# Kernel tuning notes

Measured on AMD Instinct MI355X. Metric: run time of the kernel, lower is better.

## Reference

```python
import jax, jax.numpy as jnp
import numpy as np

N, E = 50000, 800000
D_IN, D_H, D_OUT, N_LAYERS = 3, 64, 128, 3


def setup_inputs() -> dict:
    key = jax.random.key(0)
    ks = jax.random.split(key, 16)
    s = lambda k, shape, fan: jax.random.normal(k, shape, jnp.float32) * (1.0 / np.sqrt(fan))
    return {
        "x": jax.random.normal(ks[0], (N, D_IN), jnp.float32),
        "edge_index": jax.random.randint(ks[1], (2, E), 0, N, jnp.int32),
        "in_w": s(ks[2], (D_IN, D_H), D_IN),
        "in_b": jnp.zeros((D_H,), jnp.float32),
        "msg_w1": s(ks[3], (N_LAYERS, 2 * D_H, D_H), 2 * D_H),
        "msg_b1": jnp.zeros((N_LAYERS, D_H), jnp.float32),
        "msg_w2": s(ks[4], (N_LAYERS, D_H, D_H), D_H),
        "msg_b2": jnp.zeros((N_LAYERS, D_H), jnp.float32),
        "upd_w1": s(ks[5], (N_LAYERS, 2 * D_H, D_H), 2 * D_H),
        "upd_b1": jnp.zeros((N_LAYERS, D_H), jnp.float32),
        "upd_w2": s(ks[6], (N_LAYERS, D_H, D_H), D_H),
        "upd_b2": jnp.zeros((N_LAYERS, D_H), jnp.float32),
        "out_w": s(ks[7], (D_H, D_OUT), D_H),
        "out_b": jnp.zeros((D_OUT,), jnp.float32),
    }


def reference(x, edge_index, in_w, in_b, msg_w1, msg_b1, msg_w2, msg_b2,
              upd_w1, upd_b1, upd_w2, upd_b2, out_w, out_b):
    row, col = edge_index[0], edge_index[1]
    h = x @ in_w + in_b  # [N, D_H]
    for l in range(N_LAYERS):
        # gather-concat-MLP message: [E, 2*D_H] -> [E, D_H]
        msg_in = jnp.concatenate([h[row], h[col]], axis=-1)
        m = jax.nn.relu(msg_in @ msg_w1[l] + msg_b1[l]) @ msg_w2[l] + msg_b2[l]
        # scatter-add aggregation into destination nodes
        agg = jax.ops.segment_sum(m, col, num_segments=N)  # [N, D_H]
        # update MLP on concat(node, aggregated)
        upd_in = jnp.concatenate([h, agg], axis=-1)
        u = jax.nn.relu(upd_in @ upd_w1[l] + upd_b1[l]) @ upd_w2[l] + upd_b2[l]
        h = jax.nn.relu(u)
    return h @ out_w + out_b  # [N, D_OUT]
```

## Files before the change

### kernel.cpp

```cpp
#include <hip/hip_runtime.h>
#include <hip/hip_bf16.h>

#define NN 50000
#define NE 800000

typedef __bf16 bf16_t;
typedef unsigned short u16;
typedef bf16_t bf16x4 __attribute__((ext_vector_type(4)));
typedef bf16_t bf16x8 __attribute__((ext_vector_type(8)));
typedef float f32x4 __attribute__((ext_vector_type(4)));

__device__ __forceinline__ bf16x8 load_frag(const bf16_t* p) {
    bf16x4 lo = *(const bf16x4*)p;
    bf16x4 hi = *(const bf16x4*)(p + 16);
    bf16x8 f;
    f[0] = lo[0]; f[1] = lo[1]; f[2] = lo[2]; f[3] = lo[3];
    f[4] = hi[0]; f[5] = hi[1]; f[6] = hi[2]; f[7] = hi[3];
    return f;
}

__device__ __forceinline__ bf16x8 load_frag2(const bf16_t* p, const bf16_t* q) {
    bf16x8 a = load_frag(p);
    bf16x8 b = load_frag(q);
    bf16x8 f;
    #pragma unroll
    for (int j = 0; j < 8; ++j) f[j] = (bf16_t)((float)a[j] + (float)b[j]);
    return f;
}

__global__ void k_prepall(const float* __restrict__ mw1, const float* __restrict__ uw1,
                          const float* __restrict__ uw2,
                          const float* __restrict__ mw2, const float* __restrict__ mb2,
                          const float* __restrict__ ow,
                          bf16_t* __restrict__ w1t, bf16_t* __restrict__ u1t,
                          bf16_t* __restrict__ u2t,
                          bf16_t* __restrict__ w2u, float* __restrict__ cvec,
                          bf16_t* __restrict__ whi, bf16_t* __restrict__ wlo,
                          int* __restrict__ deg) {
    int gid = blockIdx.x * blockDim.x + threadIdx.x;
    int nthr = gridDim.x * blockDim.x;
    for (int i = gid; i < NN; i += nthr) deg[i] = 0;
    if (gid < 3 * 64 * 128) {
        int l = gid / 8192, r = gid % 8192, hid = r >> 7, k = r & 127;
        w1t[gid] = (bf16_t)mw1[l * 8192 + k * 64 + hid];
    }
    if (gid < 3 * 64 * 64) {
        int l = gid / 4096, r = gid % 4096, hid = r >> 6, k = r & 63;
        u1t[gid] = (bf16_t)uw1[l * 8192 + k * 64 + hid];
        u2t[gid] = (bf16_t)uw2[l * 4096 + k * 64 + hid];
        float s = 0.f;
        for (int j = 0; j < 64; ++j)
            s += mw2[l * 4096 + k * 64 + j] * uw1[l * 8192 + (64 + j) * 64 + hid];
        w2u[l * 4096 + hid * 64 + k] = (bf16_t)s;
    }
    if (gid < 3 * 64) {
        int l = gid / 64, hid = gid % 64;
        float s = 0.f;
        for (int j = 0; j < 64; ++j)
            s += mb2[l * 64 + j] * uw1[l * 8192 + (64 + j) * 64 + hid];
        cvec[gid] = s;
    }
    if (gid < 128 * 64) {
        int j = gid >> 6, k = gid & 63;
        float w = ow[k * 128 + j];
        bf16_t hi = (bf16_t)w;
        whi[gid] = hi;
        wlo[gid] = (bf16_t)(w - (float)hi);
    }
}

__global__ void k_hist(const int* __restrict__ ei, int* __restrict__ deg) {
    int gid = blockIdx.x * blockDim.x + threadIdx.x;
    if (gid < NE) atomicAdd(&deg[ei[NE + gid]], 1);
}

#define SCAN_BLKS 196
__global__ void k_scan1(const int* __restrict__ deg, int* __restrict__ tscan,
                        int* __restrict__ part) {
    __shared__ int lds[256];
    int tid = threadIdx.x;
    int gid = blockIdx.x * 256 + tid;
    int v = (gid < NN) ? deg[gid] : 0;
    lds[tid] = v;
    __syncthreads();
    for (int off = 1; off < 256; off <<= 1) {
        int t = (tid >= off) ? lds[tid - off] : 0;
        __syncthreads();
        lds[tid] += t;
        __syncthreads();
    }
    if (gid < NN) tscan[gid] = lds[tid] - v;
    if (tid == 255) part[blockIdx.x] = lds[255];
}

__global__ void k_scan23(const int* __restrict__ tscan, const int* __restrict__ part,
                         int* __restrict__ offs, int* __restrict__ cursor) {
    __shared__ int lds[256];
    int tid = threadIdx.x;
    int v = (tid < SCAN_BLKS) ? part[tid] : 0;
    lds[tid] = v;
    __syncthreads();
    for (int off = 1; off < 256; off <<= 1) {
        int t = (tid >= off) ? lds[tid - off] : 0;
        __syncthreads();
        lds[tid] += t;
        __syncthreads();
    }
    __shared__ int base;
    if (tid == 0) base = (blockIdx.x > 0) ? lds[blockIdx.x - 1] : 0;
    __syncthreads();
    int gid = blockIdx.x * 256 + tid;
    if (gid < NN) {
        int o = tscan[gid] + base;
        offs[gid] = o;
        cursor[gid] = o;
    }
    if (gid == 0) offs[NN] = NE;
}

__global__ void k_scatter(const int* __restrict__ ei, int* __restrict__ cursor,
                          u16* __restrict__ ssrc) {
    int gid = blockIdx.x * blockDim.x + threadIdx.x;
    if (gid < NE) {
        int c = ei[NE + gid];
        int pos = atomicAdd(&cursor[c], 1);
        ssrc[pos] = (u16)ei[gid];
    }
}

__global__ __launch_bounds__(256)
void k_inputpq(const float* __restrict__ x, const float* __restrict__ iw,
               const float* __restrict__ ib,
               const bf16_t* __restrict__ w1t, const float* __restrict__ b1,
               bf16_t* __restrict__ h, bf16_t* __restrict__ P, bf16_t* __restrict__ Q) {
    const int lane = threadIdx.x & 63;
    const int g = lane >> 4;
    const int m16 = lane & 15;
    const int wid = (blockIdx.x * blockDim.x + threadIdx.x) >> 6;
    const int nw = (gridDim.x * blockDim.x) >> 6;

    bf16x8 wtop[2][4], wbot[2][4];
    #pragma unroll
    for (int s = 0; s < 2; ++s)
        #pragma unroll
        for (int nt = 0; nt < 4; ++nt) {
            wtop[s][nt] = load_frag(w1t + (16 * nt + m16) * 128 + 32 * s + 4 * g);
            wbot[s][nt] = load_frag(w1t + (16 * nt + m16) * 128 + 64 + 32 * s + 4 * g);
        }
    float b1f[4][4];
    #pragma unroll
    for (int nt = 0; nt < 4; ++nt)
        #pragma unroll
        for (int r = 0; r < 4; ++r) b1f[nt][r] = b1[16 * nt + 4 * g + r];

    float wcol[3][2][8], bcol[2][8];
    #pragma unroll
    for (int s = 0; s < 2; ++s)
        #pragma unroll
        for (int j = 0; j < 8; ++j) {
            int f = 32 * s + 4 * g + (j < 4 ? j : 16 + j - 4);
            bcol[s][j] = ib[f];
            #pragma unroll
            for (int i = 0; i < 3; ++i) wcol[i][s][j] = iw[i * 64 + f];
        }

    const int ntiles = NN / 16;
    for (int t = wid; t < ntiles; t += nw) {
        const int node = t * 16 + m16;
        float x0 = x[node * 3 + 0], x1 = x[node * 3 + 1], x2 = x[node * 3 + 2];
        bf16x8 hb[2];
        #pragma unroll
        for (int s = 0; s < 2; ++s)
            #pragma unroll
            for (int j = 0; j < 8; ++j) {
                float hf = bcol[s][j] + x0 * wcol[0][s][j] + x1 * wcol[1][s][j]
                         + x2 * wcol[2][s][j];
                hb[s][j] = (bf16_t)hf;
            }
        #pragma unroll
        for (int s = 0; s < 2; ++s) {
            bf16x4 lo, hi;
            #pragma unroll
            for (int j = 0; j < 4; ++j) { lo[j] = hb[s][j]; hi[j] = hb[s][4 + j]; }
            *(bf16x4*)(h + node * 64 + 32 * s + 4 * g) = lo;
            *(bf16x4*)(h + node * 64 + 32 * s + 16 + 4 * g) = hi;
        }

        f32x4 accP[4], accQ[4];
        #pragma unroll
        for (int nt = 0; nt < 4; ++nt) {
            accP[nt] = (f32x4){0.f, 0.f, 0.f, 0.f};
            accQ[nt] = (f32x4){0.f, 0.f, 0.f, 0.f};
        }
        #pragma unroll
        for (int s = 0; s < 2; ++s)
            #pragma unroll
            for (int nt = 0; nt < 4; ++nt) {
                accP[nt] = __builtin_amdgcn_mfma_f32_16x16x32_bf16(wtop[s][nt], hb[s], accP[nt], 0, 0, 0);
                accQ[nt] = __builtin_amdgcn_mfma_f32_16x16x32_bf16(wbot[s][nt], hb[s], accQ[nt], 0, 0, 0);
            }
        #pragma unroll
        for (int nt = 0; nt < 4; ++nt) {
            bf16x4 vp, vq;
            #pragma unroll
            for (int r = 0; r < 4; ++r) {
                vp[r] = (bf16_t)accP[nt][r];
                vq[r] = (bf16_t)(accQ[nt][r] + b1f[nt][r]);
            }
            *(bf16x4*)(P + node * 64 + 16 * nt + 4 * g) = vp;
            *(bf16x4*)(Q + node * 64 + 16 * nt + 4 * g) = vq;
        }
    }
}

__global__ void k_edge(const bf16_t* __restrict__ P, const bf16_t* __restrict__ Q,
                       const u16* __restrict__ ssrc, const int* __restrict__ offs,
                       bf16_t* __restrict__ S, bf16_t* __restrict__ S2) {
    int gid = blockIdx.x * blockDim.x + threadIdx.x;
    int oct = gid >> 3, f8 = gid & 7;
    int node = oct >> 1, half = oct & 1;
    if (node >= NN) return;
    bf16x8 qv = *(const bf16x8*)(Q + node * 64 + f8 * 8);
    float qf[8], a[8];
    #pragma unroll
    for (int r = 0; r < 8; ++r) { qf[r] = (float)qv[r]; a[r] = 0.f; }
    const int b0 = offs[node], e0 = offs[node + 1];
    const int mid = b0 + ((e0 - b0 + 1) >> 1);
    const int beg = half ? mid : b0;
    const int end = half ? e0 : mid;
    int p = beg;
    const int n4 = beg + ((end - beg) & ~3);
    for (; p < n4; p += 4) {
        int s0 = ssrc[p], s1 = ssrc[p + 1], s2 = ssrc[p + 2], s3 = ssrc[p + 3];
        bf16x8 v0 = *(const bf16x8*)(P + s0 * 64 + f8 * 8);
        bf16x8 v1 = *(const bf16x8*)(P + s1 * 64 + f8 * 8);
        bf16x8 v2 = *(const bf16x8*)(P + s2 * 64 + f8 * 8);
        bf16x8 v3 = *(const bf16x8*)(P + s3 * 64 + f8 * 8);
        #pragma unroll
        for (int r = 0; r < 8; ++r) {
            float x0 = (float)v0[r] + qf[r];
            float x1 = (float)v1[r] + qf[r];
            float x2 = (float)v2[r] + qf[r];
            float x3 = (float)v3[r] + qf[r];
            a[r] += (x0 > 0.f ? x0 : 0.f) + (x1 > 0.f ? x1 : 0.f)
                  + (x2 > 0.f ? x2 : 0.f) + (x3 > 0.f ? x3 : 0.f);
        }
    }
    for (; p < end; ++p) {
        int s = ssrc[p];
        bf16x8 v = *(const bf16x8*)(P + s * 64 + f8 * 8);
        #pragma unroll
        for (int r = 0; r < 8; ++r) {
            float x = (float)v[r] + qf[r];
            a[r] += x > 0.f ? x : 0.f;
        }
    }
    bf16x8 sv;
    #pragma unroll
    for (int r = 0; r < 8; ++r) sv[r] = (bf16_t)a[r];
    bf16_t* dst = half ? S2 : S;
    *(bf16x8*)(dst + node * 64 + f8 * 8) = sv;
}

__global__ __launch_bounds__(256)
void k_updpq(const bf16_t* __restrict__ h, const bf16_t* __restrict__ S,
             const bf16_t* __restrict__ S2, const int* __restrict__ deg,
             const bf16_t* __restrict__ u1t, const bf16_t* __restrict__ w2u,
             const bf16_t* __restrict__ u2t,
             const float* __restrict__ ub1, const float* __restrict__ cvec,
             const float* __restrict__ ub2,
             const bf16_t* __restrict__ w1tn, const float* __restrict__ b1n,
             bf16_t* __restrict__ hn, bf16_t* __restrict__ P, bf16_t* __restrict__ Q) {
    const int lane = threadIdx.x & 63;
    const int g = lane >> 4;
    const int m16 = lane & 15;
    const int wid = (blockIdx.x * blockDim.x + threadIdx.x) >> 6;
    const int nw = (gridDim.x * blockDim.x) >> 6;

    bf16x8 u1f[2][4], w2f[2][4], u2f[2][4], wtop[2][4], wbot[2][4];
    #pragma unroll
    for (int s = 0; s < 2; ++s)
        #pragma unroll
        for (int nt = 0; nt < 4; ++nt) {
            u1f[s][nt] = load_frag(u1t + (16 * nt + m16) * 64 + 32 * s + 4 * g);
            w2f[s][nt] = load_frag(w2u + (16 * nt + m16) * 64 + 32 * s + 4 * g);
            u2f[s][nt] = load_frag(u2t + (16 * nt + m16) * 64 + 32 * s + 4 * g);
            wtop[s][nt] = load_frag(w1tn + (16 * nt + m16) * 128 + 32 * s + 4 * g);
            wbot[s][nt] = load_frag(w1tn + (16 * nt + m16) * 128 + 64 + 32 * s + 4 * g);
        }
    float b1f[4][4], cf[4][4], b2f[4][4], b1nf[4][4];
    #pragma unroll
    for (int nt = 0; nt < 4; ++nt)
        #pragma unroll
        for (int r = 0; r < 4; ++r) {
            b1f[nt][r] = ub1[16 * nt + 4 * g + r];
            cf[nt][r] = cvec[16 * nt + 4 * g + r];
            b2f[nt][r] = ub2[16 * nt + 4 * g + r];
            b1nf[nt][r] = b1n[16 * nt + 4 * g + r];
        }

    const int ntiles = NN / 16;
    for (int t = wid; t < ntiles; t += nw) {
        const int node = t * 16 + m16;
        bf16x8 hfr[2], sfr[2];
        hfr[0] = load_frag(h + node * 64 + 4 * g);
        hfr[1] = load_frag(h + node * 64 + 4 * g + 32);
        sfr[0] = load_frag2(S + node * 64 + 4 * g, S2 + node * 64 + 4 * g);
        sfr[1] = load_frag2(S + node * 64 + 4 * g + 32, S2 + node * 64 + 4 * g + 32);
        float dv = (float)deg[node];

        f32x4 acc1[4];
        #pragma unroll
        for (int nt = 0; nt < 4; ++nt) acc1[nt] = (f32x4){0.f, 0.f, 0.f, 0.f};
        #pragma unroll
        for (int s = 0; s < 2; ++s)
            #pragma unroll
            for (int nt = 0; nt < 4; ++nt) {
                acc1[nt] = __builtin_amdgcn_mfma_f32_16x16x32_bf16(u1f[s][nt], hfr[s], acc1[nt], 0, 0, 0);
                acc1[nt] = __builtin_amdgcn_mfma_f32_16x16x32_bf16(w2f[s][nt], sfr[s], acc1[nt], 0, 0, 0);
            }

        bf16x8 hb[2];
        #pragma unroll
        for (int s = 0; s < 2; ++s) {
            bf16x8 f;
            #pragma unroll
            for (int half = 0; half < 2; ++half) {
                const int nt = 2 * s + half;
                #pragma unroll
                for (int r = 0; r < 4; ++r) {
                    float v = acc1[nt][r] + b1f[nt][r] + dv * cf[nt][r];
                    v = v > 0.f ? v : 0.f;
                    f[4 * half + r] = (bf16_t)v;
                }
            }
            hb[s] = f;
        }

        f32x4 acc2[4];
        #pragma unroll
        for (int nt = 0; nt < 4; ++nt) acc2[nt] = (f32x4){0.f, 0.f, 0.f, 0.f};
        #pragma unroll
        for (int s = 0; s < 2; ++s)
            #pragma unroll
            for (int nt = 0; nt < 4; ++nt)
                acc2[nt] = __builtin_amdgcn_mfma_f32_16x16x32_bf16(u2f[s][nt], hb[s], acc2[nt], 0, 0, 0);

        bf16x8 hb2[2];
        #pragma unroll
        for (int s = 0; s < 2; ++s) {
            bf16x8 f;
            #pragma unroll
            for (int half = 0; half < 2; ++half) {
                const int nt = 2 * s + half;
                #pragma unroll
                for (int r = 0; r < 4; ++r) {
                    float v = acc2[nt][r] + b2f[nt][r];
                    f[4 * half + r] = (bf16_t)(v > 0.f ? v : 0.f);
                }
            }
            hb2[s] = f;
        }
        #pragma unroll
        for (int s = 0; s < 2; ++s) {
            bf16x4 lo, hi;
            #pragma unroll
            for (int j = 0; j < 4; ++j) { lo[j] = hb2[s][j]; hi[j] = hb2[s][4 + j]; }
            *(bf16x4*)(hn + node * 64 + 32 * s + 4 * g) = lo;
            *(bf16x4*)(hn + node * 64 + 32 * s + 16 + 4 * g) = hi;
        }

        f32x4 accP[4], accQ[4];
        #pragma unroll
        for (int nt = 0; nt < 4; ++nt) {
            accP[nt] = (f32x4){0.f, 0.f, 0.f, 0.f};
            accQ[nt] = (f32x4){0.f, 0.f, 0.f, 0.f};
        }
        #pragma unroll
        for (int s = 0; s < 2; ++s)
            #pragma unroll
            for (int nt = 0; nt < 4; ++nt) {
                accP[nt] = __builtin_amdgcn_mfma_f32_16x16x32_bf16(wtop[s][nt], hb2[s], accP[nt], 0, 0, 0);
                accQ[nt] = __builtin_amdgcn_mfma_f32_16x16x32_bf16(wbot[s][nt], hb2[s], accQ[nt], 0, 0, 0);
            }
        #pragma unroll
        for (int nt = 0; nt < 4; ++nt) {
            bf16x4 vp, vq;
            #pragma unroll
            for (int r = 0; r < 4; ++r) {
                vp[r] = (bf16_t)accP[nt][r];
                vq[r] = (bf16_t)(accQ[nt][r] + b1nf[nt][r]);
            }
            *(bf16x4*)(P + node * 64 + 16 * nt + 4 * g) = vp;
            *(bf16x4*)(Q + node * 64 + 16 * nt + 4 * g) = vq;
        }
    }
}

__global__ void k_upd(const bf16_t* __restrict__ h, const bf16_t* __restrict__ S,
                      const bf16_t* __restrict__ S2, const int* __restrict__ deg,
                      const bf16_t* __restrict__ u1t, const bf16_t* __restrict__ w2u,
                      const bf16_t* __restrict__ u2t,
                      const float* __restrict__ ub1, const float* __restrict__ cvec,
                      const float* __restrict__ ub2, bf16_t* __restrict__ hn) {
    const int lane = threadIdx.x & 63;
    const int g = lane >> 4;
    const int m16 = lane & 15;
    const int wid = (blockIdx.x * blockDim.x + threadIdx.x) >> 6;
    const int nw = (gridDim.x * blockDim.x) >> 6;

    bf16x8 u1f[2][4], w2f[2][4], u2f[2][4];
    #pragma unroll
    for (int s = 0; s < 2; ++s)
        #pragma unroll
        for (int nt = 0; nt < 4; ++nt) {
            u1f[s][nt] = load_frag(u1t + (16 * nt + m16) * 64 + 32 * s + 4 * g);
            w2f[s][nt] = load_frag(w2u + (16 * nt + m16) * 64 + 32 * s + 4 * g);
            u2f[s][nt] = load_frag(u2t + (16 * nt + m16) * 64 + 32 * s + 4 * g);
        }
    float b1f[4][4], cf[4][4], b2f[4][4];
    #pragma unroll
    for (int nt = 0; nt < 4; ++nt)
        #pragma unroll
        for (int r = 0; r < 4; ++r) {
            b1f[nt][r] = ub1[16 * nt + 4 * g + r];
            cf[nt][r] = cvec[16 * nt + 4 * g + r];
            b2f[nt][r] = ub2[16 * nt + 4 * g + r];
        }

    const int ntiles = NN / 16;
    for (int t = wid; t < ntiles; t += nw) {
        const int node = t * 16 + m16;
        bf16x8 hfr[2], sfr[2];
        hfr[0] = load_frag(h + node * 64 + 4 * g);
        hfr[1] = load_frag(h + node * 64 + 4 * g + 32);
        sfr[0] = load_frag2(S + node * 64 + 4 * g, S2 + node * 64 + 4 * g);
        sfr[1] = load_frag2(S + node * 64 + 4 * g + 32, S2 + node * 64 + 4 * g + 32);
        float dv = (float)deg[node];

        f32x4 acc1[4];
        #pragma unroll
        for (int nt = 0; nt < 4; ++nt) acc1[nt] = (f32x4){0.f, 0.f, 0.f, 0.f};
        #pragma unroll
        for (int s = 0; s < 2; ++s)
            #pragma unroll
            for (int nt = 0; nt < 4; ++nt) {
                acc1[nt] = __builtin_amdgcn_mfma_f32_16x16x32_bf16(u1f[s][nt], hfr[s], acc1[nt], 0, 0, 0);
                acc1[nt] = __builtin_amdgcn_mfma_f32_16x16x32_bf16(w2f[s][nt], sfr[s], acc1[nt], 0, 0, 0);
            }

        bf16x8 hb[2];
        #pragma unroll
        for (int s = 0; s < 2; ++s) {
            bf16x8 f;
            #pragma unroll
            for (int half = 0; half < 2; ++half) {
                const int nt = 2 * s + half;
                #pragma unroll
                for (int r = 0; r < 4; ++r) {
                    float v = acc1[nt][r] + b1f[nt][r] + dv * cf[nt][r];
                    v = v > 0.f ? v : 0.f;
                    f[4 * half + r] = (bf16_t)v;
                }
            }
            hb[s] = f;
        }

        f32x4 acc2[4];
        #pragma unroll
        for (int nt = 0; nt < 4; ++nt) acc2[nt] = (f32x4){0.f, 0.f, 0.f, 0.f};
        #pragma unroll
        for (int s = 0; s < 2; ++s)
            #pragma unroll
            for (int nt = 0; nt < 4; ++nt)
                acc2[nt] = __builtin_amdgcn_mfma_f32_16x16x32_bf16(u2f[s][nt], hb[s], acc2[nt], 0, 0, 0);

        #pragma unroll
        for (int nt = 0; nt < 4; ++nt) {
            bf16x4 v4;
            #pragma unroll
            for (int r = 0; r < 4; ++r) {
                float v = acc2[nt][r] + b2f[nt][r];
                v4[r] = (bf16_t)(v > 0.f ? v : 0.f);
            }
            *(bf16x4*)(hn + node * 64 + 16 * nt + 4 * g) = v4;
        }
    }
}

__global__ __launch_bounds__(256)
void k_outm(const bf16_t* __restrict__ whi_t, const bf16_t* __restrict__ wlo_t,
            const bf16_t* __restrict__ h, const float* __restrict__ b,
            float* __restrict__ out) {
    const int lane = threadIdx.x & 63;
    const int g = lane >> 4;
    const int m16 = lane & 15;
    const int wid = (blockIdx.x * blockDim.x + threadIdx.x) >> 6;
    const int nw = (gridDim.x * blockDim.x) >> 6;

    bf16x8 whi[2][8], wlo[2][8];
    #pragma unroll
    for (int s = 0; s < 2; ++s)
        #pragma unroll
        for (int nt = 0; nt < 8; ++nt) {
            whi[s][nt] = load_frag(whi_t + (16 * nt + m16) * 64 + 32 * s + 4 * g);
            wlo[s][nt] = load_frag(wlo_t + (16 * nt + m16) * 64 + 32 * s + 4 * g);
        }
    f32x4 bfv[8];
    #pragma unroll
    for (int nt = 0; nt < 8; ++nt)
        #pragma unroll
        for (int r = 0; r < 4; ++r) bfv[nt][r] = b[16 * nt + 4 * g + r];

    const int ntiles = NN / 16;
    for (int t = wid; t < ntiles; t += nw) {
        const int node = t * 16 + m16;
        bf16x8 hfr[2];
        hfr[0] = load_frag(h + node * 64 + 4 * g);
        hfr[1] = load_frag(h + node * 64 + 4 * g + 32);

        f32x4 acc[8];
        #pragma unroll
        for (int nt = 0; nt < 8; ++nt) acc[nt] = (f32x4){0.f, 0.f, 0.f, 0.f};
        #pragma unroll
        for (int s = 0; s < 2; ++s)
            #pragma unroll
            for (int nt = 0; nt < 8; ++nt) {
                acc[nt] = __builtin_amdgcn_mfma_f32_16x16x32_bf16(whi[s][nt], hfr[s], acc[nt], 0, 0, 0);
                acc[nt] = __builtin_amdgcn_mfma_f32_16x16x32_bf16(wlo[s][nt], hfr[s], acc[nt], 0, 0, 0);
            }
        #pragma unroll
        for (int nt = 0; nt < 8; ++nt)
            *(f32x4*)(out + node * 128 + 16 * nt + 4 * g) = acc[nt] + bfv[nt];
    }
}

extern "C" void kernel_launch(void* const* d_in, const int* in_sizes, int n_in,
                              void* d_out, int out_size, void* d_ws, size_t ws_size,
                              hipStream_t stream) {
    const float* x      = (const float*)d_in[0];
    const int*   ei     = (const int*)d_in[1];
    const float* in_w   = (const float*)d_in[2];
    const float* in_b   = (const float*)d_in[3];
    const float* msg_w1 = (const float*)d_in[4];
    const float* msg_b1 = (const float*)d_in[5];
    const float* msg_w2 = (const float*)d_in[6];
    const float* msg_b2 = (const float*)d_in[7];
    const float* upd_w1 = (const float*)d_in[8];
    const float* upd_b1 = (const float*)d_in[9];
    const float* upd_w2 = (const float*)d_in[10];
    const float* upd_b2 = (const float*)d_in[11];
    const float* out_w  = (const float*)d_in[12];
    const float* out_b  = (const float*)d_in[13];
    float* out = (float*)d_out;

    char* ws = (char*)d_ws;
    bf16_t* h_a    = (bf16_t*)(ws);
    bf16_t* h_b    = (bf16_t*)(ws + 6400000);
    bf16_t* P      = (bf16_t*)(ws + 12800000);
    bf16_t* Q      = (bf16_t*)(ws + 19200000);
    bf16_t* S      = (bf16_t*)(ws + 25600000);
    u16*    ssrc   = (u16*)   (ws + 32000000);
    int*    deg    = (int*)   (ws + 35200000);
    int*    offs   = (int*)   (ws + 35400000);
    int*    cursor = (int*)   (ws + 35600128);
    int*    tscan  = (int*)   (ws + 35800192);
    int*    part   = (int*)   (ws + 36000256);
    bf16_t* w1t    = (bf16_t*)(ws + 36002304);
    bf16_t* u1t    = (bf16_t*)(ws + 36051456);
    bf16_t* u2t    = (bf16_t*)(ws + 36076032);
    bf16_t* w2u    = (bf16_t*)(ws + 36100608);
    float*  cvec   = (float*) (ws + 36125184);
    bf16_t* whi    = (bf16_t*)(ws + 36126208);
    bf16_t* wlo    = (bf16_t*)(ws + 36142592);
    bf16_t* S2     = (bf16_t*)(ws + 36160000);

    k_prepall<<<96, 256, 0, stream>>>(msg_w1, upd_w1, upd_w2, msg_w2, msg_b2, out_w,
                                      w1t, u1t, u2t, w2u, cvec, whi, wlo, deg);

    k_hist<<<(NE + 255) / 256, 256, 0, stream>>>(ei, deg);
    k_scan1<<<SCAN_BLKS, 256, 0, stream>>>(deg, tscan, part);
    k_scan23<<<SCAN_BLKS, 256, 0, stream>>>(tscan, part, offs, cursor);
    k_scatter<<<(NE + 255) / 256, 256, 0, stream>>>(ei, cursor, ssrc);

    k_inputpq<<<512, 256, 0, stream>>>(x, in_w, in_b, w1t, msg_b1, h_a, P, Q);

    bf16_t* hc = h_a;
    bf16_t* hn = h_b;
    for (int l = 0; l < 3; ++l) {
        k_edge<<<(NN * 16 + 255) / 256, 256, 0, stream>>>(P, Q, ssrc, offs, S, S2);
        if (l < 2) {
            k_updpq<<<512, 256, 0, stream>>>(hc, S, S2, deg,
                u1t + l * 4096, w2u + l * 4096, u2t + l * 4096,
                upd_b1 + l * 64, cvec + l * 64, upd_b2 + l * 64,
                w1t + (l + 1) * 8192, msg_b1 + (l + 1) * 64,
                hn, P, Q);
        } else {
            k_upd<<<512, 256, 0, stream>>>(hc, S, S2, deg,
                u1t + l * 4096, w2u + l * 4096, u2t + l * 4096,
                upd_b1 + l * 64, cvec + l * 64, upd_b2 + l * 64, hn);
        }
        bf16_t* tmp = hc; hc = hn; hn = tmp;
    }
    k_outm<<<640, 256, 0, stream>>>(whi, wlo, hc, out_b, out);
}
```

Baseline: 375.5 us.

## Fuse edge aggregation into per-block update kernel via shared memory

Merges the per-node edge gather/ReLU/sum kernel with the update MLP kernel. Each 256-thread block aggregates 64 nodes into an LDS tile, then runs the MFMA update and next-layer P/Q projection on that tile. P and Q are double-buffered to avoid read/write hazards. This removes the S/S2 global round trip and one launch per layer. In exchange, each node's edges are handled by 4 threads instead of 16, weight fragments are reloaded per block, and imbalanced degrees can stall the MFMA phase.

```diff
diff --git a/kernel.cpp b/kernel.cpp
--- a/kernel.cpp
+++ b/kernel.cpp
@@ -16,15 +16,6 @@
     bf16x8 f;
     f[0] = lo[0]; f[1] = lo[1]; f[2] = lo[2]; f[3] = lo[3];
     f[4] = hi[0]; f[5] = hi[1]; f[6] = hi[2]; f[7] = hi[3];
-    return f;
-}
-
-__device__ __forceinline__ bf16x8 load_frag2(const bf16_t* p, const bf16_t* q) {
-    bf16x8 a = load_frag(p);
-    bf16x8 b = load_frag(q);
-    bf16x8 f;
-    #pragma unroll
-    for (int j = 0; j < 8; ++j) f[j] = (bf16_t)((float)a[j] + (float)b[j]);
     return f;
 }
 
@@ -213,69 +204,79 @@
     }
 }
 
-__global__ void k_edge(const bf16_t* __restrict__ P, const bf16_t* __restrict__ Q,
-                       const u16* __restrict__ ssrc, const int* __restrict__ offs,
-                       bf16_t* __restrict__ S, bf16_t* __restrict__ S2) {
-    int gid = blockIdx.x * blockDim.x + threadIdx.x;
-    int oct = gid >> 3, f8 = gid & 7;
-    int node = oct >> 1, half = oct & 1;
-    if (node >= NN) return;
-    bf16x8 qv = *(const bf16x8*)(Q + node * 64 + f8 * 8);
-    float qf[8], a[8];
-    #pragma unroll
-    for (int r = 0; r < 8; ++r) { qf[r] = (float)qv[r]; a[r] = 0.f; }
-    const int b0 = offs[node], e0 = offs[node + 1];
-    const int mid = b0 + ((e0 - b0 + 1) >> 1);
-    const int beg = half ? mid : b0;
-    const int end = half ? e0 : mid;
-    int p = beg;
-    const int n4 = beg + ((end - beg) & ~3);
-    for (; p < n4; p += 4) {
-        int s0 = ssrc[p], s1 = ssrc[p + 1], s2 = ssrc[p + 2], s3 = ssrc[p + 3];
-        bf16x8 v0 = *(const bf16x8*)(P + s0 * 64 + f8 * 8);
-        bf16x8 v1 = *(const bf16x8*)(P + s1 * 64 + f8 * 8);
-        bf16x8 v2 = *(const bf16x8*)(P + s2 * 64 + f8 * 8);
-        bf16x8 v3 = *(const bf16x8*)(P + s3 * 64 + f8 * 8);
-        #pragma unroll
-        for (int r = 0; r < 8; ++r) {
-            float x0 = (float)v0[r] + qf[r];
-            float x1 = (float)v1[r] + qf[r];
-            float x2 = (float)v2[r] + qf[r];
-            float x3 = (float)v3[r] + qf[r];
-            a[r] += (x0 > 0.f ? x0 : 0.f) + (x1 > 0.f ? x1 : 0.f)
-                  + (x2 > 0.f ? x2 : 0.f) + (x3 > 0.f ? x3 : 0.f);
-        }
-    }
-    for (; p < end; ++p) {
-        int s = ssrc[p];
-        bf16x8 v = *(const bf16x8*)(P + s * 64 + f8 * 8);
-        #pragma unroll
-        for (int r = 0; r < 8; ++r) {
-            float x = (float)v[r] + qf[r];
-            a[r] += x > 0.f ? x : 0.f;
-        }
-    }
-    bf16x8 sv;
-    #pragma unroll
-    for (int r = 0; r < 8; ++r) sv[r] = (bf16_t)a[r];
-    bf16_t* dst = half ? S2 : S;
-    *(bf16x8*)(dst + node * 64 + f8 * 8) = sv;
-}
-
 __global__ __launch_bounds__(256)
-void k_updpq(const bf16_t* __restrict__ h, const bf16_t* __restrict__ S,
-             const bf16_t* __restrict__ S2, const int* __restrict__ deg,
+void k_layer(const bf16_t* __restrict__ h, const bf16_t* __restrict__ P,
+             const bf16_t* __restrict__ Q,
+             const u16* __restrict__ ssrc, const int* __restrict__ offs,
+             const int* __restrict__ deg,
              const bf16_t* __restrict__ u1t, const bf16_t* __restrict__ w2u,
              const bf16_t* __restrict__ u2t,
              const float* __restrict__ ub1, const float* __restrict__ cvec,
              const float* __restrict__ ub2,
              const bf16_t* __restrict__ w1tn, const float* __restrict__ b1n,
-             bf16_t* __restrict__ hn, bf16_t* __restrict__ P, bf16_t* __restrict__ Q) {
-    const int lane = threadIdx.x & 63;
+             const int do_pq,
+             bf16_t* __restrict__ hn, bf16_t* __restrict__ Pn, bf16_t* __restrict__ Qn) {
+    __shared__ float Sl[64][67];
+    const int tid = threadIdx.x;
+
+    {
+        const int nl = tid >> 2;
+        const int f2 = tid & 3;
+        const int node = blockIdx.x * 64 + nl;
+        float qf[16], a[16];
+        #pragma unroll
+        for (int r = 0; r < 16; ++r) a[r] = 0.f;
+        if (node < NN) {
+            bf16x8 q0 = *(const bf16x8*)(Q + node * 64 + f2 * 16);
+            bf16x8 q1 = *(const bf16x8*)(Q + node * 64 + f2 * 16 + 8);
+            #pragma unroll
+            for (int r = 0; r < 8; ++r) { qf[r] = (float)q0[r]; qf[8 + r] = (float)q1[r]; }
+            const int beg = offs[node], end = offs[node + 1];
+            int p = beg;
+            const int n2 = beg + ((end - beg) & ~1);
+            for (; p < n2; p += 2) {
+                int s0 = ssrc[p], s1 = ssrc[p + 1];
+                const bf16_t* p0 = P + s0 * 64 + f2 * 16;
+                const bf16_t* p1 = P + s1 * 64 + f2 * 16;
+                bf16x8 v00 = *(const bf16x8*)p0;
+                bf16x8 v01 = *(const bf16x8*)(p0 + 8);
+                bf16x8 v10 = *(const bf16x8*)p1;
+                bf16x8 v11 = *(const bf16x8*)(p1 + 8);
+                #pragma unroll
+                for (int r = 0; r < 8; ++r) {
+                    float x0 = (float)v00[r] + qf[r];
+                    float x1 = (float)v10[r] + qf[r];
+                    float y0 = (float)v01[r] + qf[8 + r];
+                    float y1 = (float)v11[r] + qf[8 + r];
+                    a[r]     += (x0 > 0.f ? x0 : 0.f) + (x1 > 0.f ? x1 : 0.f);
+                    a[8 + r] += (y0 > 0.f ? y0 : 0.f) + (y1 > 0.f ? y1 : 0.f);
+                }
+            }
+            for (; p < end; ++p) {
+                int s = ssrc[p];
+                const bf16_t* pp = P + s * 64 + f2 * 16;
+                bf16x8 v0 = *(const bf16x8*)pp;
+                bf16x8 v1 = *(const bf16x8*)(pp + 8);
+                #pragma unroll
+                for (int r = 0; r < 8; ++r) {
+                    float x = (float)v0[r] + qf[r];
+                    float y = (float)v1[r] + qf[8 + r];
+                    a[r]     += x > 0.f ? x : 0.f;
+                    a[8 + r] += y > 0.f ? y : 0.f;
+                }
+            }
+        }
+        #pragma unroll
+        for (int r = 0; r < 16; ++r) Sl[nl][f2 * 16 + r] = a[r];
+    }
+    __syncthreads();
+
+    const int lane = tid & 63;
+    const int w = tid >> 6;
     const int g = lane >> 4;
     const int m16 = lane & 15;
-    const int wid = (blockIdx.x * blockDim.x + threadIdx.x) >> 6;
-    const int nw = (gridDim.x * blockDim.x) >> 6;
+    const int nl2 = w * 16 + m16;
+    const int node = blockIdx.x * 64 + nl2;
 
     bf16x8 u1f[2][4], w2f[2][4], u2f[2][4], wtop[2][4], wbot[2][4];
     #pragma unroll
@@ -285,9 +286,16 @@
             u1f[s][nt] = load_frag(u1t + (16 * nt + m16) * 64 + 32 * s + 4 * g);
             w2f[s][nt] = load_frag(w2u + (16 * nt + m16) * 64 + 32 * s + 4 * g);
             u2f[s][nt] = load_frag(u2t + (16 * nt + m16) * 64 + 32 * s + 4 * g);
-            wtop[s][nt] = load_frag(w1tn + (16 * nt + m16) * 128 + 32 * s + 4 * g);
-            wbot[s][nt] = load_frag(w1tn + (16 * nt + m16) * 128 + 64 + 32 * s + 4 * g);
-        }
+        }
+    if (do_pq) {
+        #pragma unroll
+        for (int s = 0; s < 2; ++s)
+            #pragma unroll
+            for (int nt = 0; nt < 4; ++nt) {
+                wtop[s][nt] = load_frag(w1tn + (16 * nt + m16) * 128 + 32 * s + 4 * g);
+                wbot[s][nt] = load_frag(w1tn + (16 * nt + m16) * 128 + 64 + 32 * s + 4 * g);
+            }
+    }
     float b1f[4][4], cf[4][4], b2f[4][4], b1nf[4][4];
     #pragma unroll
     for (int nt = 0; nt < 4; ++nt)
@@ -296,71 +304,77 @@
             b1f[nt][r] = ub1[16 * nt + 4 * g + r];
             cf[nt][r] = cvec[16 * nt + 4 * g + r];
             b2f[nt][r] = ub2[16 * nt + 4 * g + r];
-            b1nf[nt][r] = b1n[16 * nt + 4 * g + r];
-        }
-
-    const int ntiles = NN / 16;
-    for (int t = wid; t < ntiles; t += nw) {
-        const int node = t * 16 + m16;
-        bf16x8 hfr[2], sfr[2];
-        hfr[0] = load_frag(h + node * 64 + 4 * g);
-        hfr[1] = load_frag(h + node * 64 + 4 * g + 32);
-        sfr[0] = load_frag2(S + node * 64 + 4 * g, S2 + node * 64 + 4 * g);
-        sfr[1] = load_frag2(S + node * 64 + 4 * g + 32, S2 + node * 64 + 4 * g + 32);
-        float dv = (float)deg[node];
-
-        f32x4 acc1[4];
-        #pragma unroll
-        for (int nt = 0; nt < 4; ++nt) acc1[nt] = (f32x4){0.f, 0.f, 0.f, 0.f};
-        #pragma unroll
-        for (int s = 0; s < 2; ++s)
-            #pragma unroll
-            for (int nt = 0; nt < 4; ++nt) {
-                acc1[nt] = __builtin_amdgcn_mfma_f32_16x16x32_bf16(u1f[s][nt], hfr[s], acc1[nt], 0, 0, 0);
-                acc1[nt] = __builtin_amdgcn_mfma_f32_16x16x32_bf16(w2f[s][nt], sfr[s], acc1[nt], 0, 0, 0);
-            }
-
-        bf16x8 hb[2];
-        #pragma unroll
-        for (int s = 0; s < 2; ++s) {
-            bf16x8 f;
-            #pragma unroll
-            for (int half = 0; half < 2; ++half) {
-                const int nt = 2 * s + half;
-                #pragma unroll
-                for (int r = 0; r < 4; ++r) {
-                    float v = acc1[nt][r] + b1f[nt][r] + dv * cf[nt][r];
-                    v = v > 0.f ? v : 0.f;
-                    f[4 * half + r] = (bf16_t)v;
-                }
-            }
-            hb[s] = f;
-        }
-
-        f32x4 acc2[4];
-        #pragma unroll
-        for (int nt = 0; nt < 4; ++nt) acc2[nt] = (f32x4){0.f, 0.f, 0.f, 0.f};
-        #pragma unroll
-        for (int s = 0; s < 2; ++s)
-            #pragma unroll
-            for (int nt = 0; nt < 4; ++nt)
-                acc2[nt] = __builtin_amdgcn_mfma_f32_16x16x32_bf16(u2f[s][nt], hb[s], acc2[nt], 0, 0, 0);
-
-        bf16x8 hb2[2];
-        #pragma unroll
-        for (int s = 0; s < 2; ++s) {
-            bf16x8 f;
-            #pragma unroll
-            for (int half = 0; half < 2; ++half) {
-                const int nt = 2 * s + half;
-                #pragma unroll
-                for (int r = 0; r < 4; ++r) {
-                    float v = acc2[nt][r] + b2f[nt][r];
-                    f[4 * half + r] = (bf16_t)(v > 0.f ? v : 0.f);
-                }
-            }
-            hb2[s] = f;
-        }
+            b1nf[nt][r] = do_pq ? b1n[16 * nt + 4 * g + r] : 0.f;
+        }
+
+    bf16x8 hfr[2], sfr[2];
+    hfr[0] = load_frag(h + node * 64 + 4 * g);
+    hfr[1] = load_frag(h + node * 64 + 4 * g + 32);
+    #pragma unroll
+    for (int s = 0; s < 2; ++s) {
+        bf16x8 f;
+        #pragma unroll
+        for (int j = 0; j < 4; ++j) {
+            f[j]     = (bf16_t)Sl[nl2][32 * s + 4 * g + j];
+            f[4 + j] = (bf16_t)Sl[nl2][32 * s + 16 + 4 * g + j];
+        }
+        sfr[s] = f;
+    }
+    float dv = (float)deg[node < NN ? node : 0];
+
+    f32x4 acc1[4];
+    #pragma unroll
+    for (int nt = 0; nt < 4; ++nt) acc1[nt] = (f32x4){0.f, 0.f, 0.f, 0.f};
+    #pragma unroll
+    for (int s = 0; s < 2; ++s)
+        #pragma unroll
+        for (int nt = 0; nt < 4; ++nt) {
+            acc1[nt] = __builtin_amdgcn_mfma_f32_16x16x32_bf16(u1f[s][nt], hfr[s], acc1[nt], 0, 0, 0);
+            acc1[nt] = __builtin_amdgcn_mfma_f32_16x16x32_bf16(w2f[s][nt], sfr[s], acc1[nt], 0, 0, 0);
+        }
+
+    bf16x8 hb[2];
+    #pragma unroll
+    for (int s = 0; s < 2; ++s) {
+        bf16x8 f;
+        #pragma unroll
+        for (int half = 0; half < 2; ++half) {
+            const int nt = 2 * s + half;
+            #pragma unroll
+            for (int r = 0; r < 4; ++r) {
+                float v = acc1[nt][r] + b1f[nt][r] + dv * cf[nt][r];
+                v = v > 0.f ? v : 0.f;
+                f[4 * half + r] = (bf16_t)v;
+            }
+        }
+        hb[s] = f;
+    }
+
+    f32x4 acc2[4];
+    #pragma unroll
+    for (int nt = 0; nt < 4; ++nt) acc2[nt] = (f32x4){0.f, 0.f, 0.f, 0.f};
+    #pragma unroll
+    for (int s = 0; s < 2; ++s)
+        #pragma unroll
+        for (int nt = 0; nt < 4; ++nt)
+            acc2[nt] = __builtin_amdgcn_mfma_f32_16x16x32_bf16(u2f[s][nt], hb[s], acc2[nt], 0, 0, 0);
+
+    bf16x8 hb2[2];
+    #pragma unroll
+    for (int s = 0; s < 2; ++s) {
+        bf16x8 f;
+        #pragma unroll
+        for (int half = 0; half < 2; ++half) {
+            const int nt = 2 * s + half;
+            #pragma unroll
+            for (int r = 0; r < 4; ++r) {
+                float v = acc2[nt][r] + b2f[nt][r];
+                f[4 * half + r] = (bf16_t)(v > 0.f ? v : 0.f);
+            }
+        }
+        hb2[s] = f;
+    }
+    if (node < NN) {
         #pragma unroll
         for (int s = 0; s < 2; ++s) {
             bf16x4 lo, hi;
@@ -369,7 +383,9 @@
             *(bf16x4*)(hn + node * 64 + 32 * s + 4 * g) = lo;
             *(bf16x4*)(hn + node * 64 + 32 * s + 16 + 4 * g) = hi;
         }
-
+    }
+
+    if (do_pq) {
         f32x4 accP[4], accQ[4];
         #pragma unroll
         for (int nt = 0; nt < 4; ++nt) {
@@ -383,107 +399,18 @@
                 accP[nt] = __builtin_amdgcn_mfma_f32_16x16x32_bf16(wtop[s][nt], hb2[s], accP[nt], 0, 0, 0);
                 accQ[nt] = __builtin_amdgcn_mfma_f32_16x16x32_bf16(wbot[s][nt], hb2[s], accQ[nt], 0, 0, 0);
             }
-        #pragma unroll
-        for (int nt = 0; nt < 4; ++nt) {
-            bf16x4 vp, vq;
-            #pragma unroll
-            for (int r = 0; r < 4; ++r) {
-                vp[r] = (bf16_t)accP[nt][r];
-                vq[r] = (bf16_t)(accQ[nt][r] + b1nf[nt][r]);
-            }
-            *(bf16x4*)(P + node * 64 + 16 * nt + 4 * g) = vp;
-            *(bf16x4*)(Q + node * 64 + 16 * nt + 4 * g) = vq;
-        }
-    }
-}
-
-__global__ void k_upd(const bf16_t* __restrict__ h, const bf16_t* __restrict__ S,
-                      const bf16_t* __restrict__ S2, const int* __restrict__ deg,
-                      const bf16_t* __restrict__ u1t, const bf16_t* __restrict__ w2u,
-                      const bf16_t* __restrict__ u2t,
-                      const float* __restrict__ ub1, const float* __restrict__ cvec,
-                      const float* __restrict__ ub2, bf16_t* __restrict__ hn) {
-    const int lane = threadIdx.x & 63;
-    const int g = lane >> 4;
-    const int m16 = lane & 15;
-    const int wid = (blockIdx.x * blockDim.x + threadIdx.x) >> 6;
-    const int nw = (gridDim.x * blockDim.x) >> 6;
-
-    bf16x8 u1f[2][4], w2f[2][4], u2f[2][4];
-    #pragma unroll
-    for (int s = 0; s < 2; ++s)
-        #pragma unroll
-        for (int nt = 0; nt < 4; ++nt) {
-            u1f[s][nt] = load_frag(u1t + (16 * nt + m16) * 64 + 32 * s + 4 * g);
-            w2f[s][nt] = load_frag(w2u + (16 * nt + m16) * 64 + 32 * s + 4 * g);
-            u2f[s][nt] = load_frag(u2t + (16 * nt + m16) * 64 + 32 * s + 4 * g);
-        }
-    float b1f[4][4], cf[4][4], b2f[4][4];
-    #pragma unroll
-    for (int nt = 0; nt < 4; ++nt)
-        #pragma unroll
-        for (int r = 0; r < 4; ++r) {
-            b1f[nt][r] = ub1[16 * nt + 4 * g + r];
-            cf[nt][r] = cvec[16 * nt + 4 * g + r];
-            b2f[nt][r] = ub2[16 * nt + 4 * g + r];
-        }
-
-    const int ntiles = NN / 16;
-    for (int t = wid; t < ntiles; t += nw) {
-        const int node = t * 16 + m16;
-        bf16x8 hfr[2], sfr[2];
-        hfr[0] = load_frag(h + node * 64 + 4 * g);
-        hfr[1] = load_frag(h + node * 64 + 4 * g + 32);
-        sfr[0] = load_frag2(S + node * 64 + 4 * g, S2 + node * 64 + 4 * g);
-        sfr[1] = load_frag2(S + node * 64 + 4 * g + 32, S2 + node * 64 + 4 * g + 32);
-        float dv = (float)deg[node];
-
-        f32x4 acc1[4];
-        #pragma unroll
-        for (int nt = 0; nt < 4; ++nt) acc1[nt] = (f32x4){0.f, 0.f, 0.f, 0.f};
-        #pragma unroll
-        for (int s = 0; s < 2; ++s)
+        if (node < NN) {
             #pragma unroll
             for (int nt = 0; nt < 4; ++nt) {
-                acc1[nt] = __builtin_amdgcn_mfma_f32_16x16x32_bf16(u1f[s][nt], hfr[s], acc1[nt], 0, 0, 0);
-                acc1[nt] = __builtin_amdgcn_mfma_f32_16x16x32_bf16(w2f[s][nt], sfr[s], acc1[nt], 0, 0, 0);
-            }
-
-        bf16x8 hb[2];
-        #pragma unroll
-        for (int s = 0; s < 2; ++s) {
-            bf16x8 f;
-            #pragma unroll
-            for (int half = 0; half < 2; ++half) {
-                const int nt = 2 * s + half;
+                bf16x4 vp, vq;
                 #pragma unroll
                 for (int r = 0; r < 4; ++r) {
-                    float v = acc1[nt][r] + b1f[nt][r] + dv * cf[nt][r];
-                    v = v > 0.f ? v : 0.f;
-                    f[4 * half + r] = (bf16_t)v;
+                    vp[r] = (bf16_t)accP[nt][r];
+                    vq[r] = (bf16_t)(accQ[nt][r] + b1nf[nt][r]);
                 }
-            }
-            hb[s] = f;
-        }
-
-        f32x4 acc2[4];
-        #pragma unroll
-        for (int nt = 0; nt < 4; ++nt) acc2[nt] = (f32x4){0.f, 0.f, 0.f, 0.f};
-        #pragma unroll
-        for (int s = 0; s < 2; ++s)
-            #pragma unroll
-            for (int nt = 0; nt < 4; ++nt)
-                acc2[nt] = __builtin_amdgcn_mfma_f32_16x16x32_bf16(u2f[s][nt], hb[s], acc2[nt], 0, 0, 0);
-
-        #pragma unroll
-        for (int nt = 0; nt < 4; ++nt) {
-            bf16x4 v4;
-            #pragma unroll
-            for (int r = 0; r < 4; ++r) {
-                float v = acc2[nt][r] + b2f[nt][r];
-                v4[r] = (bf16_t)(v > 0.f ? v : 0.f);
-            }
-            *(bf16x4*)(hn + node * 64 + 16 * nt + 4 * g) = v4;
+                *(bf16x4*)(Pn + node * 64 + 16 * nt + 4 * g) = vp;
+                *(bf16x4*)(Qn + node * 64 + 16 * nt + 4 * g) = vq;
+            }
         }
     }
 }
@@ -557,9 +484,9 @@
     char* ws = (char*)d_ws;
     bf16_t* h_a    = (bf16_t*)(ws);
     bf16_t* h_b    = (bf16_t*)(ws + 6400000);
-    bf16_t* P      = (bf16_t*)(ws + 12800000);
-    bf16_t* Q      = (bf16_t*)(ws + 19200000);
-    bf16_t* S      = (bf16_t*)(ws + 25600000);
+    bf16_t* Pa     = (bf16_t*)(ws + 12800000);
+    bf16_t* Qa     = (bf16_t*)(ws + 19200000);
+    bf16_t* Pb     = (bf16_t*)(ws + 25600000);
     u16*    ssrc   = (u16*)   (ws + 32000000);
     int*    deg    = (int*)   (ws + 35200000);
     int*    offs   = (int*)   (ws + 35400000);
@@ -573,7 +500,7 @@
     float*  cvec   = (float*) (ws + 36125184);
     bf16_t* whi    = (bf16_t*)(ws + 36126208);
     bf16_t* wlo    = (bf16_t*)(ws + 36142592);
-    bf16_t* S2     = (bf16_t*)(ws + 36160000);
+    bf16_t* Qb     = (bf16_t*)(ws + 36160000);
 
     k_prepall<<<96, 256, 0, stream>>>(msg_w1, upd_w1, upd_w2, msg_w2, msg_b2, out_w,
                                       w1t, u1t, u2t, w2u, cvec, whi, wlo, deg);
@@ -583,24 +510,24 @@
     k_scan23<<<SCAN_BLKS, 256, 0, stream>>>(tscan, part, offs, cursor);
     k_scatter<<<(NE + 255) / 256, 256, 0, stream>>>(ei, cursor, ssrc);
 
-    k_inputpq<<<512, 256, 0, stream>>>(x, in_w, in_b, w1t, msg_b1, h_a, P, Q);
-
-    bf16_t* hc = h_a;
-    bf16_t* hn = h_b;
+    k_inputpq<<<512, 256, 0, stream>>>(x, in_w, in_b, w1t, msg_b1, h_a, Pa, Qa);
+
+    const int NB = (NN + 63) / 64;
+    bf16_t* hc = h_a; bf16_t* hn = h_b;
+    bf16_t* Pc = Pa;  bf16_t* Qc = Qa;
+    bf16_t* Pn = Pb;  bf16_t* Qn = Qb;
     for (int l = 0; l < 3; ++l) {
-        k_edge<<<(NN * 16 + 255) / 256, 256, 0, stream>>>(P, Q, ssrc, offs, S, S2);
-        if (l < 2) {
-            k_updpq<<<512, 256, 0, stream>>>(hc, S, S2, deg,
-                u1t + l * 4096, w2u + l * 4096, u2t + l * 4096,
-                upd_b1 + l * 64, cvec + l * 64, upd_b2 + l * 64,
-                w1t + (l + 1) * 8192, msg_b1 + (l + 1) * 64,
-                hn, P, Q);
-        } else {
-            k_upd<<<512, 256, 0, stream>>>(hc, S, S2, deg,
-                u1t + l * 4096, w2u + l * 4096, u2t + l * 4096,
-                upd_b1 + l * 64, cvec + l * 64, upd_b2 + l * 64, hn);
-        }
-        bf16_t* tmp = hc; hc = hn; hn = tmp;
+        int do_pq = (l < 2) ? 1 : 0;
+        const bf16_t* w1tn = do_pq ? (w1t + (l + 1) * 8192) : w1t;
+        const float*  b1n  = do_pq ? (msg_b1 + (l + 1) * 64) : msg_b1;
+        k_layer<<<NB, 256, 0, stream>>>(hc, Pc, Qc, ssrc, offs, deg,
+                                        u1t + l * 4096, w2u + l * 4096, u2t + l * 4096,
+                                        upd_b1 + l * 64, cvec + l * 64, upd_b2 + l * 64,
+                                        w1tn, b1n, do_pq, hn, Pn, Qn);
+        bf16_t* t;
+        t = hc; hc = hn; hn = t;
+        t = Pc; Pc = Pn; Pn = t;
+        t = Qc; Qc = Qn; Qn = t;
     }
     k_outm<<<640, 256, 0, stream>>>(whi, wlo, hc, out_b, out);
 }
```

Measured after the change: 468.7 us. +24.8%, slower.
